# Optimization experiments

Hardware: AMD Instinct MI355X
Metric: run time of the kernel (lower is better)

## Reference

```python
import jax, jax.numpy as jnp
import numpy as np

N_NODES = 100000
N_EDGES = 3200000
IN_DIM, HID, OUT_DIM = 1, 64, 1


def graph_conv(x, src, dst, ew, W_rel, b_rel, W_root):
    # PyG GraphConv (aggr='add'): out_i = W_rel @ sum_{j->i} w_ij x_j + b_rel + W_root @ x_i
    msg = x[src] * ew[:, None]                               # [E, F]
    agg = jax.ops.segment_sum(msg, dst, num_segments=N_NODES)  # [N, F]
    return agg @ W_rel + b_rel + x @ W_root


def setup_inputs() -> dict:
    key = jax.random.key(0)
    ks = jax.random.split(key, 12)
    def glorot(k, shape):
        fan_in, fan_out = shape
        lim = float(np.sqrt(6.0 / (fan_in + fan_out)))
        return jax.random.uniform(k, shape, jnp.float32, -lim, lim)
    x = jax.random.normal(ks[0], (N_NODES, IN_DIM), jnp.float32)
    edge_index = jax.random.randint(ks[1], (2, N_EDGES), 0, N_NODES, jnp.int64)
    edge_weight = jax.random.uniform(ks[2], (N_EDGES,), jnp.float32)
    return {
        "x": x, "edge_index": edge_index, "edge_weight": edge_weight,
        "W1_rel": glorot(ks[3], (IN_DIM, HID)), "b1": jnp.zeros((HID,), jnp.float32),
        "W1_root": glorot(ks[4], (IN_DIM, HID)),
        "W2_rel": glorot(ks[5], (HID, HID)), "b2": jnp.zeros((HID,), jnp.float32),
        "W2_root": glorot(ks[6], (HID, HID)),
        "W3_rel": glorot(ks[7], (HID, OUT_DIM)), "b3": jnp.zeros((OUT_DIM,), jnp.float32),
        "W3_root": glorot(ks[8], (HID, OUT_DIM)),
    }


def reference(x, edge_index, edge_weight, W1_rel, b1, W1_root, W2_rel, b2, W2_root, W3_rel, b3, W3_root):
    src, dst = edge_index[0], edge_index[1]
    h = graph_conv(x, src, dst, edge_weight, W1_rel, b1, W1_root)
    h = jax.nn.relu(h)  # dropout is identity in eval mode
    h = graph_conv(h, src, dst, edge_weight, W2_rel, b2, W2_root)
    h = jax.nn.relu(h)
    return graph_conv(h, src, dst, edge_weight, W3_rel, b3, W3_root)
```

## Files before the change

kernel.cpp:

```cpp
#include <hip/hip_runtime.h>

#define NN 100000
#define NE 3200000
#define HID 64
#define NPB 256
#define NB  ((NN + NPB - 1) / NPB)
#define NNP (NB * NPB)
#define CAP 9216
#define MNP 128
#define NMW (2 * NB)
#define WNP 64
#define NW2 (NNP / WNP)
#define CAPW 5120
#define CHUNK 4096
#define NCH ((NE + CHUNK - 1) / CHUNK)
#define AP 72
#define BPITCH 136
#define SRCM 0x1FFFF

typedef _Float16 half8 __attribute__((ext_vector_type(8)));
typedef _Float16 h2v   __attribute__((ext_vector_type(2)));
typedef float f32x4 __attribute__((ext_vector_type(4)));

__device__ __forceinline__ unsigned short f2hb(float v) {
    _Float16 h = (_Float16)v;
    unsigned short s;
    __builtin_memcpy(&s, &h, 2);
    return s;
}
__device__ __forceinline__ float h2f(unsigned int u) {
    unsigned short s = (unsigned short)u;
    _Float16 h;
    __builtin_memcpy(&h, &s, 2);
    return (float)h;
}
__device__ __forceinline__ h2v ash2(unsigned int u) {
    h2v r;
    __builtin_memcpy(&r, &u, 4);
    return r;
}

__global__ __launch_bounds__(512) void k_init(const float* __restrict__ x,
                                              float2* __restrict__ sx,
                                              int* __restrict__ deg,
                                              int* __restrict__ gcur) {
    const int i = blockIdx.x * 512 + threadIdx.x;
    if (i < NN) sx[i] = make_float2(0.f, x[i]);
    if (i < NNP) deg[i] = 0;
    if (blockIdx.x == 0 && threadIdx.x < NB) gcur[threadIdx.x] = threadIdx.x * CAP;
}

__global__ __launch_bounds__(512) void k_scatter(const int* __restrict__ src,
                                                 const int* __restrict__ dst,
                                                 const float* __restrict__ ew,
                                                 int* __restrict__ gcur,
                                                 int* __restrict__ rec_a,
                                                 unsigned short* __restrict__ rec_w) {
    __shared__ int la[CHUNK];
    __shared__ unsigned short lw[CHUNK];
    __shared__ unsigned short lb[CHUNK];
    __shared__ unsigned short sidx[CHUNK];
    __shared__ int cnt[NB];
    __shared__ int bme[NB];
    __shared__ int wt8[8];
    const int tid = threadIdx.x;
    const int lane = tid & 63, wvx = tid >> 6;
    for (int j = tid; j < NB; j += 512) cnt[j] = 0;
    __syncthreads();
    const long long b0 = (long long)blockIdx.x * CHUNK;
    const int valid = (int)min((long long)CHUNK, (long long)NE - b0);
    if (valid == CHUNK) {
        int dd[CHUNK / 512], ss[CHUNK / 512];
        float ww[CHUNK / 512];
        #pragma unroll
        for (int k = 0; k < CHUNK / 512; ++k) {
            const long long e = b0 + k * 512 + tid;
            dd[k] = dst[e]; ss[k] = src[e]; ww[k] = ew[e];
        }
        #pragma unroll
        for (int k = 0; k < CHUNK / 512; ++k) {
            const int idx = k * 512 + tid;
            const int d = dd[k];
            const int b = d >> 8;
            la[idx] = ss[k] | ((d & 255) << 17);
            lw[idx] = f2hb(ww[k]);
            lb[idx] = (unsigned short)b;
            atomicAdd(&cnt[b], 1);
        }
    } else {
        #pragma unroll
        for (int k = 0; k < CHUNK / 512; ++k) {
            int idx = k * 512 + tid;
            if (idx < valid) {
                long long e = b0 + idx;
                int d = dst[e];
                int b = d >> 8;
                la[idx] = src[e] | ((d & 255) << 17);
                lw[idx] = f2hb(ew[e]);
                lb[idx] = (unsigned short)b;
                atomicAdd(&cnt[b], 1);
            }
        }
    }
    __syncthreads();
    const int v = (tid < NB) ? cnt[tid] : 0;
    int incl = v;
    #pragma unroll
    for (int off = 1; off < 64; off <<= 1) {
        int t0 = __shfl_up(incl, off, 64);
        if (lane >= off) incl += t0;
    }
    if (lane == 63) wt8[wvx] = incl;
    __syncthreads();
    int offs = 0;
    #pragma unroll
    for (int j = 0; j < 8; ++j)
        if (j < wvx) offs += wt8[j];
    const int excl = offs + incl - v;
    if (tid < NB) {
        int bb = v ? atomicAdd(&gcur[tid], v) : 0;
        bme[tid] = bb - excl;
        cnt[tid] = excl;
    }
    __syncthreads();
    #pragma unroll
    for (int k = 0; k < CHUNK / 512; ++k) {
        int idx = k * 512 + tid;
        if (idx < valid) {
            int sp = atomicAdd(&cnt[lb[idx]], 1);
            sidx[sp] = (unsigned short)idx;
        }
    }
    __syncthreads();
    #pragma unroll
    for (int k = 0; k < CHUNK / 512; ++k) {
        int sp = k * 512 + tid;
        if (sp < valid) {
            int idx = sidx[sp];
            int b = lb[idx];
            int go = bme[b] + sp;
            rec_a[go] = la[idx];
            rec_w[go] = lw[idx];
        }
    }
}

__global__ __launch_bounds__(512) void k_s1(const int* __restrict__ gcur,
                                            const int* __restrict__ rec_a,
                                            const unsigned short* __restrict__ rec_w,
                                            const float* __restrict__ x,
                                            float* __restrict__ sxf,
                                            int* __restrict__ deg) {
    __shared__ float loc[NPB];
    __shared__ int ideg[NPB];
    if (threadIdx.x < NPB) { loc[threadIdx.x] = 0.f; ideg[threadIdx.x] = 0; }
    __syncthreads();
    const int wid = blockIdx.x;
    const int b = wid >> 2, j = wid & 3;
    const int beg = b * CAP, cnt = gcur[b] - beg;
    const int qtr = ((cnt + 15) >> 4) << 2;
    const int lo = min(cnt, j * qtr);
    const int hi = min(cnt, lo + qtr);
    const int n = hi - lo;
    const int n4 = n >> 2;
    const int4* a4 = (const int4*)(rec_a + beg + lo);
    const ushort4* w4 = (const ushort4*)(rec_w + beg + lo);
    for (int t = threadIdx.x; t < n4; t += 512) {
        const int4 qa = a4[t];
        const ushort4 qw = w4[t];
        const float g0 = x[qa.x & SRCM], g1 = x[qa.y & SRCM];
        const float g2 = x[qa.z & SRCM], g3 = x[qa.w & SRCM];
        atomicAdd(&loc[qa.x >> 17], h2f(qw.x) * g0);
        atomicAdd(&loc[qa.y >> 17], h2f(qw.y) * g1);
        atomicAdd(&loc[qa.z >> 17], h2f(qw.z) * g2);
        atomicAdd(&loc[qa.w >> 17], h2f(qw.w) * g3);
        atomicAdd(&ideg[qa.x >> 17], 1);
        atomicAdd(&ideg[qa.y >> 17], 1);
        atomicAdd(&ideg[qa.z >> 17], 1);
        atomicAdd(&ideg[qa.w >> 17], 1);
    }
    for (int t = beg + lo + (n4 << 2) + threadIdx.x; t < beg + hi; t += 512) {
        const int a = rec_a[t];
        atomicAdd(&loc[a >> 17], h2f(rec_w[t]) * x[a & SRCM]);
        atomicAdd(&ideg[a >> 17], 1);
    }
    __syncthreads();
    const int i = b * NPB + threadIdx.x;
    if (threadIdx.x < NPB) {
        float vv = loc[threadIdx.x];
        if (vv != 0.f && i < NN) atomicAdd(&sxf[2 * i], vv);
        int dv = ideg[threadIdx.x];
        if (dv) atomicAdd(&deg[i], dv);
    }
}

__global__ __launch_bounds__(512) void k_pack(const int* __restrict__ gcur,
                                              const int* __restrict__ deg,
                                              const int* __restrict__ rec_a,
                                              const unsigned short* __restrict__ rec_w,
                                              const float2* __restrict__ sx,
                                              unsigned short* __restrict__ rec2s,
                                              unsigned short* __restrict__ rec2x,
                                              unsigned short* __restrict__ rec2f,
                                              int* __restrict__ noff,
                                              unsigned char* __restrict__ ngrp) {
    __shared__ int4 imgq[3 * CAPW / 8];
    __shared__ int exclp[128];
    __shared__ int cur[128];
    __shared__ int wt2[2];
    unsigned short* img = (unsigned short*)imgq;
    unsigned short* ws_img = img;
    unsigned short* wx_img = img + CAPW;
    unsigned short* wf_img = img + 2 * CAPW;
    const int tid = threadIdx.x;
    const int lane = tid & 63, wv = tid >> 6;
    const int wid = blockIdx.x;
    const int b = wid >> 1, h = wid & 1;
    for (int j = tid; j < 3 * CAPW / 8; j += 512) imgq[j] = (int4){0, 0, 0, 0};
    __syncthreads();
    const int beg = b * CAP;
    const int cnt = gcur[b] - beg;
    int pc = 0, incl = 0;
    if (tid < 128) { pc = (deg[wid * MNP + tid] + 7) & ~7; incl = pc; }
    #pragma unroll
    for (int off = 1; off < 64; off <<= 1) {
        int tt = __shfl_up(incl, off, 64);
        if (lane >= off) incl += tt;
    }
    if (tid < 128 && lane == 63) wt2[wv] = incl;
    __syncthreads();
    if (tid < 128) {
        int e0 = ((tid >= 64) ? wt2[0] : 0) + incl - pc;
        exclp[tid] = e0;
        cur[tid] = e0;
        const int node = wid * MNP + tid;
        noff[node] = wid * CAPW + e0;
        ngrp[node] = (unsigned char)(pc >> 3);
    }
    __syncthreads();
#define PREC(AA, WW) {                                                  \
        const int dl_ = (AA) >> 17;                                     \
        if ((dl_ >> 7) == h) {                                          \
            const float w_ = h2f(WW);                                   \
            const float2 v_ = sx[(AA) & SRCM];                          \
            int gs_ = atomicAdd(&cur[dl_ & 127], 1);                    \
            ws_img[gs_] = f2hb(w_ * v_.x);                              \
            wx_img[gs_] = f2hb(w_ * v_.y);                              \
            wf_img[gs_] = (unsigned short)(WW);                         \
        } }
    {
        const int4* a4 = (const int4*)(rec_a + beg);
        const ushort4* w4 = (const ushort4*)(rec_w + beg);
        const int n4 = cnt >> 2;
        for (int t = tid; t < n4; t += 512) {
            int4 qa = a4[t];
            ushort4 qw = w4[t];
            PREC(qa.x, qw.x)
            PREC(qa.y, qw.y)
            PREC(qa.z, qw.z)
            PREC(qa.w, qw.w)
        }
        for (int t = (n4 << 2) + tid; t < cnt; t += 512) {
            PREC(rec_a[beg + t], rec_w[beg + t])
        }
    }
#undef PREC
    __syncthreads();
    {
        const size_t pb = (size_t)wid * (CAPW / 8);
        int4* d0 = (int4*)rec2s + pb;
        int4* d1 = (int4*)rec2x + pb;
        int4* d2 = (int4*)rec2f + pb;
        for (int j = tid; j < CAPW / 8; j += 512) d0[j] = imgq[j];
        for (int j = tid; j < CAPW / 8; j += 512) d1[j] = imgq[CAPW / 8 + j];
        for (int j = tid; j < CAPW / 8; j += 512) d2[j] = imgq[2 * (CAPW / 8) + j];
    }
}

__global__ __launch_bounds__(512) void k_mega(
        const int* __restrict__ noff, const unsigned char* __restrict__ ngrp,
        const unsigned short* __restrict__ rec2s,
        const unsigned short* __restrict__ rec2x,
        const unsigned short* __restrict__ rec2f,
        const float2* __restrict__ sx,
        const float* __restrict__ W1_rel, const float* __restrict__ W1_root,
        const float* __restrict__ b1,
        const float* __restrict__ W2_rel, const float* __restrict__ b2,
        const float* __restrict__ W2_root,
        const float* __restrict__ W3_rel, const float* __restrict__ W3_root,
        const float* __restrict__ b3,
        float* __restrict__ p, float* __restrict__ out) {
    __shared__ _Float16 aggh[WNP * AP];
    __shared__ _Float16 Bt[HID * BPITCH];
    __shared__ float2 sxl[WNP];
    __shared__ float partP[2][WNP];
    __shared__ float partR[2][WNP];
    const int tid = threadIdx.x;
    const int f = tid & 63;
    const int wv = tid >> 6;
    const int gi0 = blockIdx.x * WNP;

    for (int j = tid; j < WNP * AP / 2; j += 512) ((int*)aggh)[j] = 0;
    for (int idx = tid; idx < HID * HID; idx += 512) {
        int k = idx >> 6, n = idx & 63;
        Bt[n * BPITCH + k]       = (_Float16)W2_rel[idx];
        Bt[n * BPITCH + HID + k] = (_Float16)W2_root[idx];
    }
    if (tid < WNP) {
        int gi = gi0 + tid;
        sxl[tid] = (gi < NN) ? sx[gi] : make_float2(0.f, 0.f);
    }
    const float w1rf = W1_rel[f], w1tf = W1_root[f], b1ff = b1[f];
    const float b3v = b3[0];
    __syncthreads();

    {
        const int first = gi0 + wv * 8;
        int soff = __builtin_amdgcn_readfirstlane(noff[first]);
        const int2 gv = *(const int2*)(ngrp + first);
        unsigned ua = __builtin_amdgcn_readfirstlane((unsigned)gv.x);
        unsigned ub = __builtin_amdgcn_readfirstlane((unsigned)gv.y);
        unsigned long long clo = (unsigned long long)ua | ((unsigned long long)ub << 32);
        #define BSUM(u) (((u) & 255u) + (((u) >> 8) & 255u) + (((u) >> 16) & 255u) + ((u) >> 24))
        const int tg = (int)(BSUM(ua) + BSUM(ub));
        #undef BSUM

        const h2v w1r2 = {(_Float16)w1rf, (_Float16)w1rf};
        const h2v w1t2 = {(_Float16)w1tf, (_Float16)w1tf};
        const h2v b1f2 = {(_Float16)b1ff, (_Float16)b1ff};
        const h2v one2 = {(_Float16)1.f, (_Float16)1.f};
        const h2v zero2 = {(_Float16)0.f, (_Float16)0.f};

        float a0 = 0.f, a1 = 0.f, a2 = 0.f, a3 = 0.f;
        int nrow = wv * 8;
        const int rowend = nrow + 8;
        int grem = (int)(clo & 255); clo >>= 8;
        while (grem == 0 && nrow + 1 < rowend) {
            ++nrow; grem = (int)(clo & 255); clo >>= 8;
        }

        const int4* ps = (const int4*)rec2s + (soff >> 3);
        const int4* px = (const int4*)rec2x + (soff >> 3);
        const int4* pf = (const int4*)rec2f + (soff >> 3);

        int4 S0, X0, F0, S1, X1, F1, S2, X2, F2, S3, X3, F3;
        if (tg >= 1) { S0 = ps[0]; X0 = px[0]; F0 = pf[0]; }
        if (tg >= 2) { S1 = ps[1]; X1 = px[1]; F1 = pf[1]; }
        if (tg >= 3) { S2 = ps[2]; X2 = px[2]; F2 = pf[2]; }

#define PP(SS, XX, FF, AA) {                                 \
        h2v z_ = ash2((unsigned)(FF)) * b1f2;                \
        z_ = ash2((unsigned)(XX)) * w1t2 + z_;               \
        z_ = ash2((unsigned)(SS)) * w1r2 + z_;               \
        z_ = __builtin_elementwise_max(z_, zero2);           \
        AA = __builtin_amdgcn_fdot2(z_, one2, AA, false); }

#define GRP(S, X, F)                                         \
        PP(S.x, X.x, F.x, a0) PP(S.y, X.y, F.y, a1)          \
        PP(S.z, X.z, F.z, a2) PP(S.w, X.w, F.w, a3)

#define BNDRY() {                                                        \
        if (--grem == 0) {                                               \
            aggh[nrow * AP + f] = (_Float16)((a0 + a1) + (a2 + a3));     \
            a0 = a1 = a2 = a3 = 0.f;                                     \
            ++nrow; grem = (int)(clo & 255); clo >>= 8;                  \
            while (grem == 0 && nrow + 1 < rowend) {                     \
                ++nrow; grem = (int)(clo & 255); clo >>= 8;              \
            }                                                            \
        } }

        int t = 0;
        while (t + 4 <= tg) {
            S3 = ps[t + 3]; X3 = px[t + 3]; F3 = pf[t + 3];
            GRP(S0, X0, F0) BNDRY(); ++t;
            S0 = ps[t + 3]; X0 = px[t + 3]; F0 = pf[t + 3];
            GRP(S1, X1, F1) BNDRY(); ++t;
            S1 = ps[t + 3]; X1 = px[t + 3]; F1 = pf[t + 3];
            GRP(S2, X2, F2) BNDRY(); ++t;
            S2 = ps[t + 3]; X2 = px[t + 3]; F2 = pf[t + 3];
            GRP(S3, X3, F3) BNDRY(); ++t;
        }
        if (t < tg) {
            GRP(S0, X0, F0) BNDRY(); ++t;
            if (t < tg) {
                GRP(S1, X1, F1) BNDRY(); ++t;
                if (t < tg) {
                    GRP(S2, X2, F2) BNDRY(); ++t;
                }
            }
        }
#undef PP
#undef GRP
#undef BNDRY
    }
    __syncthreads();

    const int m16 = tid & 15;
    const int quad = (tid & 63) >> 4;
    const int rw = wv & 3;
    const int cw = wv >> 2;
    f32x4 acc[2];
    acc[0] = (f32x4){0.f, 0.f, 0.f, 0.f};
    acc[1] = (f32x4){0.f, 0.f, 0.f, 0.f};

    const float2 sm = sxl[rw * 16 + m16];

    #pragma unroll
    for (int kt = 0; kt < 4; ++kt) {
        const int kk = kt * 32;
        half8 af;
        if (kt < 2) {
            af = *(const half8*)&aggh[(rw * 16 + m16) * AP + kk + quad * 8];
        } else {
            const int fk0 = (kt - 2) * 32 + quad * 8;
            #pragma unroll
            for (int j = 0; j < 8; ++j) {
                const float wr = W1_rel[fk0 + j], wt = W1_root[fk0 + j], bb = b1[fk0 + j];
                af[j] = (_Float16)fmaxf(0.f, fmaf(sm.x, wr, fmaf(sm.y, wt, bb)));
            }
        }
        #pragma unroll
        for (int c = 0; c < 2; ++c) {
            const int ct = cw * 2 + c;
            const half8 bfrag = *(const half8*)&Bt[(ct * 16 + m16) * BPITCH + kk + quad * 8];
            acc[c] = __builtin_amdgcn_mfma_f32_16x16x32_f16(af, bfrag, acc[c], 0, 0, 0);
        }
    }

    float b2c[2], w3rc[2], w3tc[2];
    #pragma unroll
    for (int c = 0; c < 2; ++c) {
        const int col = (cw * 2 + c) * 16 + m16;
        b2c[c] = b2[col]; w3rc[c] = W3_rel[col]; w3tc[c] = W3_root[col];
    }
    float pv[4] = {0.f, 0.f, 0.f, 0.f}, rv[4] = {0.f, 0.f, 0.f, 0.f};
    #pragma unroll
    for (int c = 0; c < 2; ++c) {
        #pragma unroll
        for (int reg = 0; reg < 4; ++reg) {
            const float h2_ = fmaxf(0.f, acc[c][reg] + b2c[c]);
            pv[reg] = fmaf(h2_, w3rc[c], pv[reg]);
            rv[reg] = fmaf(h2_, w3tc[c], rv[reg]);
        }
    }
    #pragma unroll
    for (int reg = 0; reg < 4; ++reg) {
        #pragma unroll
        for (int msk = 1; msk < 16; msk <<= 1) {
            pv[reg] += __shfl_xor(pv[reg], msk, 64);
            rv[reg] += __shfl_xor(rv[reg], msk, 64);
        }
    }
    if (m16 == 0) {
        #pragma unroll
        for (int reg = 0; reg < 4; ++reg) {
            const int row = rw * 16 + quad * 4 + reg;
            partP[cw][row] = pv[reg];
            partR[cw][row] = rv[reg];
        }
    }
    __syncthreads();
    if (tid < WNP) {
        const int gi = gi0 + tid;
        if (gi < NN) {
            p[gi]   = partP[0][tid] + partP[1][tid];
            out[gi] = partR[0][tid] + partR[1][tid] + b3v;
        }
    }
}

__global__ __launch_bounds__(512) void k_out(const int* __restrict__ gcur,
                                             const int* __restrict__ rec_a,
                                             const unsigned short* __restrict__ rec_w,
                                             const float* __restrict__ pp,
                                             float* __restrict__ out) {
    __shared__ float loc[NPB];
    if (threadIdx.x < NPB) loc[threadIdx.x] = 0.f;
    __syncthreads();
    const int wid = blockIdx.x;
    const int b = wid >> 2, j = wid & 3;
    const int beg = b * CAP, cnt = gcur[b] - beg;
    const int qtr = ((cnt + 15) >> 4) << 2;
    const int lo = min(cnt, j * qtr);
    const int hi = min(cnt, lo + qtr);
    const int n = hi - lo;
    const int n4 = n >> 2;
    const int4* a4 = (const int4*)(rec_a + beg + lo);
    const ushort4* w4 = (const ushort4*)(rec_w + beg + lo);
    for (int t = threadIdx.x; t < n4; t += 512) {
        const int4 qa = a4[t];
        const ushort4 qw = w4[t];
        const float g0 = pp[qa.x & SRCM], g1 = pp[qa.y & SRCM];
        const float g2 = pp[qa.z & SRCM], g3 = pp[qa.w & SRCM];
        atomicAdd(&loc[qa.x >> 17], h2f(qw.x) * g0);
        atomicAdd(&loc[qa.y >> 17], h2f(qw.y) * g1);
        atomicAdd(&loc[qa.z >> 17], h2f(qw.z) * g2);
        atomicAdd(&loc[qa.w >> 17], h2f(qw.w) * g3);
    }
    for (int t = beg + lo + (n4 << 2) + threadIdx.x; t < beg + hi; t += 512) {
        const int a = rec_a[t];
        atomicAdd(&loc[a >> 17], h2f(rec_w[t]) * pp[a & SRCM]);
    }
    __syncthreads();
    const int i = b * NPB + threadIdx.x;
    if (threadIdx.x < NPB && i < NN) {
        float v = loc[threadIdx.x];
        if (v != 0.f) atomicAdd(&out[i], v);
    }
}

extern "C" void kernel_launch(void* const* d_in, const int* in_sizes, int n_in,
                              void* d_out, int out_size, void* d_ws, size_t ws_size,
                              hipStream_t stream) {
    const float* x       = (const float*)d_in[0];
    const int*   ei      = (const int*)  d_in[1];
    const float* ew      = (const float*)d_in[2];
    const float* W1_rel  = (const float*)d_in[3];
    const float* b1      = (const float*)d_in[4];
    const float* W1_root = (const float*)d_in[5];
    const float* W2_rel  = (const float*)d_in[6];
    const float* b2      = (const float*)d_in[7];
    const float* W2_root = (const float*)d_in[8];
    const float* W3_rel  = (const float*)d_in[9];
    const float* b3      = (const float*)d_in[10];
    const float* W3_root = (const float*)d_in[11];

    const int* src = ei;
    const int* dst = ei + NE;

    const size_t REC_SLOTS = (size_t)NB * CAP;
    const size_t PLANE     = (size_t)NMW * CAPW;
    int*            rec_a = (int*)d_ws;
    unsigned short* rec_w = (unsigned short*)(rec_a + REC_SLOTS);
    float2*         sx    = (float2*)(rec_w + REC_SLOTS);
    float*          p     = (float*)(sx + NN);
    int*            noff  = (int*)(p + NN);
    unsigned char*  ngrp  = (unsigned char*)(noff + NNP);
    int*            deg   = (int*)(ngrp + NNP);
    int*            gcur  = deg + NNP;
    char*           tail  = (char*)(gcur + NB);
    size_t          off   = ((size_t)(tail - (char*)d_ws) + 15) & ~(size_t)15;
    unsigned short* rec2s = (unsigned short*)((char*)d_ws + off);
    unsigned short* rec2x = rec2s + PLANE;
    unsigned short* rec2f = rec2x + PLANE;

    k_init<<<(NNP + 511) / 512, 512, 0, stream>>>(x, sx, deg, gcur);
    k_scatter<<<NCH, 512, 0, stream>>>(src, dst, ew, gcur, rec_a, rec_w);
    k_s1<<<4 * NB, 512, 0, stream>>>(gcur, rec_a, rec_w, x, (float*)sx, deg);
    k_pack<<<NMW, 512, 0, stream>>>(gcur, deg, rec_a, rec_w, sx,
                                    rec2s, rec2x, rec2f, noff, ngrp);
    k_mega<<<NW2, 512, 0, stream>>>(noff, ngrp, rec2s, rec2x, rec2f, sx,
                                    W1_rel, W1_root, b1,
                                    W2_rel, b2, W2_root,
                                    W3_rel, W3_root, b3, p, (float*)d_out);
    k_out<<<4 * NB, 512, 0, stream>>>(gcur, rec_a, rec_w, p, (float*)d_out);
}
```

Before: 233.6 us.

## Split each bucket across eight blocks, simplify scatter loads, interleave pack stores

Each destination bucket in k_s1 and k_out is now split into eighths instead of quarters, doubling the grid so more blocks run with shorter per-block loops. In k_scatter the separate full-chunk path, which batched all global loads into registers before the LDS writes, is removed in favour of the single bounds-checked loop. The k_pack write-back now reads all three shared-memory planes and then stores them in one loop instead of three. More blocks mean more partial atomic flushes to global memory, and dropping the batched loads may reduce memory-level parallelism in the scatter kernel.

```diff
diff --git a/kernel.cpp b/kernel.cpp
--- a/kernel.cpp
+++ b/kernel.cpp
@@ -69,37 +69,17 @@
     __syncthreads();
     const long long b0 = (long long)blockIdx.x * CHUNK;
     const int valid = (int)min((long long)CHUNK, (long long)NE - b0);
-    if (valid == CHUNK) {
-        int dd[CHUNK / 512], ss[CHUNK / 512];
-        float ww[CHUNK / 512];
-        #pragma unroll
-        for (int k = 0; k < CHUNK / 512; ++k) {
-            const long long e = b0 + k * 512 + tid;
-            dd[k] = dst[e]; ss[k] = src[e]; ww[k] = ew[e];
-        }
-        #pragma unroll
-        for (int k = 0; k < CHUNK / 512; ++k) {
-            const int idx = k * 512 + tid;
-            const int d = dd[k];
-            const int b = d >> 8;
-            la[idx] = ss[k] | ((d & 255) << 17);
-            lw[idx] = f2hb(ww[k]);
+    #pragma unroll
+    for (int k = 0; k < CHUNK / 512; ++k) {
+        int idx = k * 512 + tid;
+        if (idx < valid) {
+            long long e = b0 + idx;
+            int d = dst[e];
+            int b = d >> 8;
+            la[idx] = src[e] | ((d & 255) << 17);
+            lw[idx] = f2hb(ew[e]);
             lb[idx] = (unsigned short)b;
             atomicAdd(&cnt[b], 1);
-        }
-    } else {
-        #pragma unroll
-        for (int k = 0; k < CHUNK / 512; ++k) {
-            int idx = k * 512 + tid;
-            if (idx < valid) {
-                long long e = b0 + idx;
-                int d = dst[e];
-                int b = d >> 8;
-                la[idx] = src[e] | ((d & 255) << 17);
-                lw[idx] = f2hb(ew[e]);
-                lb[idx] = (unsigned short)b;
-                atomicAdd(&cnt[b], 1);
-            }
         }
     }
     __syncthreads();
@@ -156,11 +136,11 @@
     if (threadIdx.x < NPB) { loc[threadIdx.x] = 0.f; ideg[threadIdx.x] = 0; }
     __syncthreads();
     const int wid = blockIdx.x;
-    const int b = wid >> 2, j = wid & 3;
+    const int b = wid >> 3, j = wid & 7;
     const int beg = b * CAP, cnt = gcur[b] - beg;
-    const int qtr = ((cnt + 15) >> 4) << 2;
-    const int lo = min(cnt, j * qtr);
-    const int hi = min(cnt, lo + qtr);
+    const int oct = ((cnt + 31) >> 5) << 2;
+    const int lo = min(cnt, j * oct);
+    const int hi = min(cnt, lo + oct);
     const int n = hi - lo;
     const int n4 = n >> 2;
     const int4* a4 = (const int4*)(rec_a + beg + lo);
@@ -271,9 +251,12 @@
         int4* d0 = (int4*)rec2s + pb;
         int4* d1 = (int4*)rec2x + pb;
         int4* d2 = (int4*)rec2f + pb;
-        for (int j = tid; j < CAPW / 8; j += 512) d0[j] = imgq[j];
-        for (int j = tid; j < CAPW / 8; j += 512) d1[j] = imgq[CAPW / 8 + j];
-        for (int j = tid; j < CAPW / 8; j += 512) d2[j] = imgq[2 * (CAPW / 8) + j];
+        for (int j = tid; j < CAPW / 8; j += 512) {
+            const int4 v0 = imgq[j];
+            const int4 v1 = imgq[CAPW / 8 + j];
+            const int4 v2 = imgq[2 * (CAPW / 8) + j];
+            d0[j] = v0; d1[j] = v1; d2[j] = v2;
+        }
     }
 }
 
@@ -478,11 +461,11 @@
     if (threadIdx.x < NPB) loc[threadIdx.x] = 0.f;
     __syncthreads();
     const int wid = blockIdx.x;
-    const int b = wid >> 2, j = wid & 3;
+    const int b = wid >> 3, j = wid & 7;
     const int beg = b * CAP, cnt = gcur[b] - beg;
-    const int qtr = ((cnt + 15) >> 4) << 2;
-    const int lo = min(cnt, j * qtr);
-    const int hi = min(cnt, lo + qtr);
+    const int oct = ((cnt + 31) >> 5) << 2;
+    const int lo = min(cnt, j * oct);
+    const int hi = min(cnt, lo + oct);
     const int n = hi - lo;
     const int n4 = n >> 2;
     const int4* a4 = (const int4*)(rec_a + beg + lo);
@@ -546,12 +529,12 @@
 
     k_init<<<(NNP + 511) / 512, 512, 0, stream>>>(x, sx, deg, gcur);
     k_scatter<<<NCH, 512, 0, stream>>>(src, dst, ew, gcur, rec_a, rec_w);
-    k_s1<<<4 * NB, 512, 0, stream>>>(gcur, rec_a, rec_w, x, (float*)sx, deg);
+    k_s1<<<8 * NB, 512, 0, stream>>>(gcur, rec_a, rec_w, x, (float*)sx, deg);
     k_pack<<<NMW, 512, 0, stream>>>(gcur, deg, rec_a, rec_w, sx,
                                     rec2s, rec2x, rec2f, noff, ngrp);
     k_mega<<<NW2, 512, 0, stream>>>(noff, ngrp, rec2s, rec2x, rec2f, sx,
                                     W1_rel, W1_root, b1,
                                     W2_rel, b2, W2_root,
                                     W3_rel, W3_root, b3, p, (float*)d_out);
-    k_out<<<4 * NB, 512, 0, stream>>>(gcur, rec_a, rec_w, p, (float*)d_out);
-}
+    k_out<<<8 * NB, 512, 0, stream>>>(gcur, rec_a, rec_w, p, (float*)d_out);
+}
```

Measured after the change: 235.3 us. Within noise of the previous version (+0.7%).
